# Kernel tuning notes

Hardware: AMD Instinct MI355X
Metric: run time of the kernel (lower is better)

The kernel has to match this reference:

```python
import jax, jax.numpy as jnp
import numpy as np

B, S, H = 2, 2048, 2048
NH, HD = 16, 128


def _rope_tables(seq_len, dim, base=10000.0):
    inv_freq = 1.0 / (base ** (np.arange(0, dim, 2, dtype=np.float32) / dim))
    t = np.arange(seq_len, dtype=np.float32)
    freqs = np.outer(t, inv_freq)                      # [S, dim/2]
    emb = np.concatenate([freqs, freqs], axis=-1)      # [S, dim] (HF convention)
    return jnp.asarray(np.cos(emb)), jnp.asarray(np.sin(emb))


def setup_inputs() -> dict:
    key = jax.random.key(0)
    k1, k2, k3, k4, k5 = jax.random.split(key, 5)
    hidden_states = jax.random.normal(k1, (B, S, H), dtype=jnp.float32)
    # additive causal mask, broadcast over heads: (B, 1, S, S)
    causal = jnp.tril(jnp.ones((S, S), dtype=bool))
    attention_mask = jnp.where(causal, 0.0, -1e9).astype(jnp.float32)
    attention_mask = jnp.broadcast_to(attention_mask[None, None], (B, 1, S, S))
    rope_cos, rope_sin = _rope_tables(S, HD)
    scale = 1.0 / np.sqrt(H)
    Wq = jax.random.normal(k2, (H, H), dtype=jnp.float32) * scale
    Wk = jax.random.normal(k3, (H, H), dtype=jnp.float32) * scale
    Wv = jax.random.normal(k4, (H, H), dtype=jnp.float32) * scale
    Wo = jax.random.normal(k5, (H, H), dtype=jnp.float32) * scale
    return dict(hidden_states=hidden_states, attention_mask=attention_mask,
                rope_cos=rope_cos, rope_sin=rope_sin, Wq=Wq, Wk=Wk, Wv=Wv, Wo=Wo)


def _rotate_half(x):
    half = x.shape[-1] // 2
    return jnp.concatenate([-x[..., half:], x[..., :half]], axis=-1)


def reference(hidden_states, attention_mask, rope_cos, rope_sin, Wq, Wk, Wv, Wo):
    bsz, q_len, _ = hidden_states.shape
    scaling = HD ** -0.5
    # projections (torch Linear: y = x @ W.T)
    q = (hidden_states @ Wq.T).reshape(bsz, q_len, NH, HD).transpose(0, 2, 1, 3)
    k = (hidden_states @ Wk.T).reshape(bsz, q_len, NH, HD).transpose(0, 2, 1, 3)
    v = (hidden_states @ Wv.T).reshape(bsz, q_len, NH, HD).transpose(0, 2, 1, 3)
    # RoPE (rotate_half convention)
    cos = rope_cos[None, None]  # [1,1,S,HD]
    sin = rope_sin[None, None]
    q = q * cos + _rotate_half(q) * sin
    k = k * cos + _rotate_half(k) * sin
    # attention
    scores = jnp.einsum('bhqd,bhkd->bhqk', q, k) * scaling + attention_mask
    attn = jax.nn.softmax(scores.astype(jnp.float32), axis=-1).astype(q.dtype)
    out = jnp.einsum('bhqk,bhkd->bhqd', attn, v)
    out = out.transpose(0, 2, 1, 3).reshape(bsz, q_len, NH * HD)
    return out @ Wo.T
```

## Files before the change

### kernel.cpp

```cpp
#include <hip/hip_runtime.h>
#include <hip/hip_bf16.h>

typedef __bf16 bf16;
typedef __attribute__((ext_vector_type(8))) __bf16 bf16x8;
typedef __attribute__((ext_vector_type(4))) __bf16 bf16x4;
typedef __attribute__((ext_vector_type(4))) float f32x4;

#define BB 2
#define SS 2048
#define HH 2048
#define NH 16
#define HD 128

#define GLOAD_LDS16(g, l)                                                  \
    __builtin_amdgcn_global_load_lds(                                      \
        (const __attribute__((address_space(1))) void*)(g),                \
        (__attribute__((address_space(3))) void*)(l), 16, 0, 0)

__global__ __launch_bounds__(256) void cast_all(const float* __restrict__ hs,
                                                const float* __restrict__ Wq,
                                                const float* __restrict__ Wk,
                                                const float* __restrict__ Wv,
                                                const float* __restrict__ Wo,
                                                bf16* __restrict__ Xb,
                                                bf16* __restrict__ Wqkv,
                                                bf16* __restrict__ Wob) {
    const int XE4 = (BB * SS * HH) / 4;
    const int WE4 = (HH * HH) / 4;
    int i = blockIdx.x * 256 + threadIdx.x;
    const float* src;
    bf16* dst;
    int off;
    if (i < XE4) { src = hs; dst = Xb; off = i; }
    else if (i < XE4 + WE4) { src = Wq; dst = Wqkv; off = i - XE4; }
    else if (i < XE4 + 2 * WE4) { src = Wk; dst = Wqkv + (size_t)HH * HH; off = i - XE4 - WE4; }
    else if (i < XE4 + 3 * WE4) { src = Wv; dst = Wqkv + 2 * (size_t)HH * HH; off = i - XE4 - 2 * WE4; }
    else { src = Wo; dst = Wob; off = i - XE4 - 3 * WE4; }
    f32x4 v = *reinterpret_cast<const f32x4*>(src + (size_t)off * 4);
    bf16x4 o;
    o[0] = (bf16)v[0]; o[1] = (bf16)v[1]; o[2] = (bf16)v[2]; o[3] = (bf16)v[3];
    *reinterpret_cast<bf16x4*>(dst + (size_t)off * 4) = o;
}

__global__ __launch_bounds__(512, 2) void gemm256_qkv(const bf16* __restrict__ A,
                                                      const bf16* __restrict__ B,
                                                      bf16* __restrict__ Cb,
                                                      int M, int N, int K) {
    __shared__ bf16 LA[2][256 * 64];
    __shared__ bf16 LB[2][256 * 64];
    const int tid = threadIdx.x, lane = tid & 63, wave = tid >> 6;
    const int l15 = lane & 15, lhi = lane >> 4;
    const int wr = wave >> 2, wc = wave & 3;
    const int NBY = M >> 8;
    const int cpx = gridDim.x >> 3;
    const int wg = (blockIdx.x & 7) * cpx + (blockIdx.x >> 3);
    const int m0 = (wg % NBY) * 256, n0 = (wg / NBY) * 256;
    const int NK = K >> 6;
    const int xorR = (l15 & 7) << 4;

    auto stageA = [&](int buf, int t, int h) {
        const int k0 = t << 6;
#pragma unroll
        for (int j = 0; j < 2; ++j) {
            int Xw = ((j * 128 + h * 64) << 7) + (wave << 10);
            int X = Xw + lane * 16;
            int T = X ^ (((X >> 7) & 7) << 4);
            GLOAD_LDS16(&A[(size_t)(m0 + (T >> 7)) * K + k0 + ((T & 127) >> 1)],
                        (char*)LA[buf] + Xw);
        }
    };
    auto stageB = [&](int buf, int t, int h) {
        const int k0 = t << 6;
#pragma unroll
        for (int j = 0; j < 2; ++j) {
            int base_row = h * 32 + (2 * j + (wave >> 2)) * 64;
            int Xw = (base_row << 7) + ((wave & 3) << 10);
            int X = Xw + lane * 16;
            int T = X ^ (((X >> 7) & 7) << 4);
            GLOAD_LDS16(&B[(size_t)(n0 + (T >> 7)) * K + k0 + ((T & 127) >> 1)],
                        (char*)LB[buf] + Xw);
        }
    };

    f32x4 acc[8][4] = {};

    stageA(0, 0, 0); stageB(0, 0, 0); stageB(0, 0, 1); stageA(0, 0, 1);
    stageA(1, 1, 0); stageB(1, 1, 1);
    asm volatile("s_waitcnt vmcnt(4)" ::: "memory");
    __builtin_amdgcn_s_barrier();

    bf16x8 af[4][2], bv0[2][2], bv1[2][2];

#pragma unroll 1
    for (int t = 0; t < NK; ++t) {
        const int buf = t & 1;
        char* lA = (char*)LA[buf];
        char* lB = (char*)LB[buf];

#pragma unroll
        for (int f = 0; f < 4; ++f)
#pragma unroll
            for (int ks = 0; ks < 2; ++ks) {
                int T = ((wr * 128 + f * 16 + l15) << 7) + ks * 64 + lhi * 16;
                af[f][ks] = *reinterpret_cast<const bf16x8*>(lA + (T ^ xorR));
            }
#pragma unroll
        for (int g = 0; g < 2; ++g)
#pragma unroll
            for (int ks = 0; ks < 2; ++ks) {
                int T = ((wc * 64 + g * 16 + l15) << 7) + ks * 64 + lhi * 16;
                bv0[g][ks] = *reinterpret_cast<const bf16x8*>(lB + (T ^ xorR));
            }
        if (t + 1 < NK) stageB(buf ^ 1, t + 1, 0);
        __builtin_amdgcn_s_barrier();
        __builtin_amdgcn_s_setprio(1);
#pragma unroll
        for (int f = 0; f < 4; ++f)
#pragma unroll
            for (int g = 0; g < 2; ++g)
#pragma unroll
                for (int ks = 0; ks < 2; ++ks)
                    acc[f][g] = __builtin_amdgcn_mfma_f32_16x16x32_bf16(af[f][ks], bv0[g][ks], acc[f][g], 0, 0, 0);
        __builtin_amdgcn_s_setprio(0);
        __builtin_amdgcn_s_barrier();

#pragma unroll
        for (int g = 0; g < 2; ++g)
#pragma unroll
            for (int ks = 0; ks < 2; ++ks) {
                int T = ((wc * 64 + 32 + g * 16 + l15) << 7) + ks * 64 + lhi * 16;
                bv1[g][ks] = *reinterpret_cast<const bf16x8*>(lB + (T ^ xorR));
            }
        if (t + 1 < NK) stageA(buf ^ 1, t + 1, 1);
        __builtin_amdgcn_s_barrier();
        __builtin_amdgcn_s_setprio(1);
#pragma unroll
        for (int f = 0; f < 4; ++f)
#pragma unroll
            for (int g = 0; g < 2; ++g)
#pragma unroll
                for (int ks = 0; ks < 2; ++ks)
                    acc[f][2 + g] = __builtin_amdgcn_mfma_f32_16x16x32_bf16(af[f][ks], bv1[g][ks], acc[f][2 + g], 0, 0, 0);
        __builtin_amdgcn_s_setprio(0);
        __builtin_amdgcn_s_barrier();

#pragma unroll
        for (int f = 0; f < 4; ++f)
#pragma unroll
            for (int ks = 0; ks < 2; ++ks) {
                int T = ((wr * 128 + 64 + f * 16 + l15) << 7) + ks * 64 + lhi * 16;
                af[f][ks] = *reinterpret_cast<const bf16x8*>(lA + (T ^ xorR));
            }
        if (t + 2 < NK) stageA(buf, t + 2, 0);
        __builtin_amdgcn_s_barrier();
        __builtin_amdgcn_s_setprio(1);
#pragma unroll
        for (int f = 0; f < 4; ++f)
#pragma unroll
            for (int g = 0; g < 2; ++g)
#pragma unroll
                for (int ks = 0; ks < 2; ++ks)
                    acc[4 + f][2 + g] = __builtin_amdgcn_mfma_f32_16x16x32_bf16(af[f][ks], bv1[g][ks], acc[4 + f][2 + g], 0, 0, 0);
        __builtin_amdgcn_s_setprio(0);
        __builtin_amdgcn_s_barrier();

        if (t + 2 < NK) stageB(buf, t + 2, 1);
        __builtin_amdgcn_s_barrier();
        __builtin_amdgcn_s_setprio(1);
#pragma unroll
        for (int f = 0; f < 4; ++f)
#pragma unroll
            for (int g = 0; g < 2; ++g)
#pragma unroll
                for (int ks = 0; ks < 2; ++ks)
                    acc[4 + f][g] = __builtin_amdgcn_mfma_f32_16x16x32_bf16(af[f][ks], bv0[g][ks], acc[4 + f][g], 0, 0, 0);
        __builtin_amdgcn_s_setprio(0);
        if (t + 2 == NK) {
            asm volatile("s_waitcnt vmcnt(0)" ::: "memory");
        } else if (t + 1 < NK) {
            asm volatile("s_waitcnt vmcnt(4)" ::: "memory");
        }
        __builtin_amdgcn_s_barrier();
    }

#pragma unroll
    for (int mf = 0; mf < 8; ++mf)
#pragma unroll
        for (int nf = 0; nf < 4; ++nf)
#pragma unroll
            for (int r = 0; r < 4; ++r) {
                int gm = m0 + wr * 128 + mf * 16 + lhi * 4 + r;
                int gn = n0 + wc * 64 + nf * 16 + l15;
                int proj = gn >> 11, n2 = gn & 2047;
                int b = gm >> 11, s = gm & (SS - 1);
                int h = n2 >> 7, d = n2 & (HD - 1);
                Cb[((size_t)proj << 23) + ((((size_t)(b * NH + h)) * SS + s) << 7) + d] =
                    (bf16)acc[mf][nf][r];
            }
}

__global__ __launch_bounds__(256) void gemm_bt(const bf16* __restrict__ A,
                                               const bf16* __restrict__ B,
                                               float* __restrict__ Cf,
                                               int M, int N, int K) {
    __shared__ bf16 As[128 * 64];
    __shared__ bf16 Bs[128 * 64];
    const int tid = threadIdx.x;
    const int lane = tid & 63, wave = tid >> 6;
    const int l15 = lane & 15, lhi = lane >> 4;
    const int m0 = blockIdx.y * 128, n0 = blockIdx.x * 128;
    const int wm = (wave >> 1) * 64, wn = (wave & 1) * 64;
    const int lrow = lane >> 3;
    const int lcol = (lane & 7) * 8;

    f32x4 acc[4][4] = {};

    for (int k0 = 0; k0 < K; k0 += 64) {
#pragma unroll
        for (int j = 0; j < 4; ++j) {
            const int c = wave * 4 + j;
            const int row = c * 8 + lrow;
            GLOAD_LDS16(&A[(size_t)(m0 + row) * K + k0 + lcol], &As[c * 512]);
            GLOAD_LDS16(&B[(size_t)(n0 + row) * K + k0 + lcol], &Bs[c * 512]);
        }
        __syncthreads();
#pragma unroll
        for (int ks = 0; ks < 2; ++ks) {
            bf16x8 af[4], bfr[4];
#pragma unroll
            for (int i = 0; i < 4; ++i)
                af[i] = *reinterpret_cast<const bf16x8*>(&As[(wm + i * 16 + l15) * 64 + ks * 32 + 8 * lhi]);
#pragma unroll
            for (int j = 0; j < 4; ++j)
                bfr[j] = *reinterpret_cast<const bf16x8*>(&Bs[(wn + j * 16 + l15) * 64 + ks * 32 + 8 * lhi]);
#pragma unroll
            for (int i = 0; i < 4; ++i)
#pragma unroll
                for (int j = 0; j < 4; ++j)
                    acc[i][j] = __builtin_amdgcn_mfma_f32_16x16x32_bf16(af[i], bfr[j], acc[i][j], 0, 0, 0);
        }
        __syncthreads();
    }

#pragma unroll
    for (int i = 0; i < 4; ++i)
#pragma unroll
        for (int j = 0; j < 4; ++j)
#pragma unroll
            for (int r = 0; r < 4; ++r) {
                int gm = m0 + wm + i * 16 + lhi * 4 + r;
                int gn = n0 + wn + j * 16 + l15;
                Cf[(size_t)gm * N + gn] = acc[i][j][r];
            }
}

__global__ __launch_bounds__(256) void rope_tv(bf16* __restrict__ Qh,
                                               bf16* __restrict__ Kh,
                                               const float* __restrict__ cosT,
                                               const float* __restrict__ sinT,
                                               const bf16* __restrict__ Vh,
                                               bf16* __restrict__ Vt) {
    __shared__ bf16 T[64 * 64];
    const int tid = threadIdx.x;
    if (blockIdx.x < 2048) {
        int idx = blockIdx.x * 256 + tid;
        int g = idx & 7;
        int s = (idx >> 3) & (SS - 1);
        int head = idx >> 14;
        int d0 = g * 8;
        size_t base = ((size_t)head * SS + s) * HD;
        f32x4 ca = *reinterpret_cast<const f32x4*>(&cosT[s * HD + d0]);
        f32x4 cb = *reinterpret_cast<const f32x4*>(&cosT[s * HD + d0 + 4]);
        f32x4 sa = *reinterpret_cast<const f32x4*>(&sinT[s * HD + d0]);
        f32x4 sb = *reinterpret_cast<const f32x4*>(&sinT[s * HD + d0 + 4]);
        bf16x8 ql = *reinterpret_cast<const bf16x8*>(&Qh[base + d0]);
        bf16x8 qh = *reinterpret_cast<const bf16x8*>(&Qh[base + 64 + d0]);
        bf16x8 kl = *reinterpret_cast<const bf16x8*>(&Kh[base + d0]);
        bf16x8 kh = *reinterpret_cast<const bf16x8*>(&Kh[base + 64 + d0]);
        bf16x8 qlo, qhi, klo, khi;
#pragma unroll
        for (int j = 0; j < 8; ++j) {
            float c = (j < 4) ? ca[j] : cb[j - 4];
            float sn = (j < 4) ? sa[j] : sb[j - 4];
            float q0 = (float)ql[j], q1 = (float)qh[j];
            float k0 = (float)kl[j], k1 = (float)kh[j];
            qlo[j] = (bf16)(q0 * c - q1 * sn);
            qhi[j] = (bf16)(q1 * c + q0 * sn);
            klo[j] = (bf16)(k0 * c - k1 * sn);
            khi[j] = (bf16)(k1 * c + k0 * sn);
        }
        *reinterpret_cast<bf16x8*>(&Qh[base + d0]) = qlo;
        *reinterpret_cast<bf16x8*>(&Qh[base + 64 + d0]) = qhi;
        *reinterpret_cast<bf16x8*>(&Kh[base + d0]) = klo;
        *reinterpret_cast<bf16x8*>(&Kh[base + 64 + d0]) = khi;
    } else {
        const int b2 = blockIdx.x - 2048;
        const int s0 = (b2 & 31) * 64;
        const int d0 = ((b2 >> 5) & 1) * 64;
        const int head = b2 >> 6;
        const bf16* src = Vh + ((size_t)head * SS) * HD;
        bf16* dst = Vt + ((size_t)head * HD) * SS;

#pragma unroll
        for (int i = 0; i < 2; ++i) {
            int id = tid + i * 256;
            int r = id >> 3, c16 = id & 7;
            bf16x8 v = *reinterpret_cast<const bf16x8*>(&src[(size_t)(s0 + r) * HD + d0 + c16 * 8]);
            int sw = c16 ^ ((r ^ (r >> 3)) & 7);
            *reinterpret_cast<bf16x8*>((char*)T + r * 128 + sw * 16) = v;
        }
        __syncthreads();
#pragma unroll
        for (int i = 0; i < 2; ++i) {
            int id = tid + i * 256;
            int dr = id >> 3, sc8 = (id & 7) * 8;
            bf16x8 o;
#pragma unroll
            for (int j = 0; j < 8; ++j) {
                int r = sc8 + j;
                int sw = (dr >> 3) ^ ((r ^ (r >> 3)) & 7);
                o[j] = *reinterpret_cast<const bf16*>((char*)T + r * 128 + sw * 16 + (dr & 7) * 2);
            }
            *reinterpret_cast<bf16x8*>(&dst[(size_t)(d0 + dr) * SS + s0 + sc8]) = o;
        }
    }
}

__global__ __launch_bounds__(512) void attn_kernel(const bf16* __restrict__ Q,
                                                   const bf16* __restrict__ K,
                                                   const bf16* __restrict__ Vt,
                                                   bf16* __restrict__ Ob) {
    __shared__ bf16 Ks[2][64 * 128];
    __shared__ bf16 Vs[2][128 * 64];
    __shared__ bf16 Ps[8][16 * 72];

    const int tid = threadIdx.x, lane = tid & 63, wave = tid >> 6;
    const int l15 = lane & 15, lhi = lane >> 4;
    const int bid = blockIdx.x;
    const int orig = (bid & 7) * 32 + (bid >> 3);
    const int head = orig >> 3;
    const int pi = orig & 7;
    const int b = head >> 4, h = head & (NH - 1);
    const size_t hb = (size_t)head * SS * HD;
    const bf16* Vth = Vt + (size_t)head * HD * SS;
    const float cexp = 0.08838834764831845f * 1.4426950408889634f;
    const float THR = 62.0f;

    auto stageKV = [&](int buf, int kv0) {
#pragma unroll
        for (int j = 0; j < 2; ++j) {
            int Xw = (j * 8 + wave) << 10;
            int X = Xw + lane * 16;
            int T = X ^ (((X >> 8) & 7) << 4);
            GLOAD_LDS16(&K[hb + (size_t)(kv0 + (T >> 8)) * HD + ((T & 255) >> 1)],
                        (char*)Ks[buf] + Xw);
        }
#pragma unroll
        for (int j = 0; j < 2; ++j) {
            int Xw = (j * 8 + wave) << 10;
            int X = Xw + lane * 16;
            int T = X ^ (((X >> 7) & 7) << 4);
            GLOAD_LDS16(&Vth[(size_t)(T >> 7) * SS + kv0 + ((T & 127) >> 1)],
                        (char*)Vs[buf] + Xw);
        }
    };

#pragma unroll 1
    for (int part = 0; part < 2; ++part) {
        const int t = part ? (15 - pi) : pi;
        const int q0 = t * 128;
        const int qw = q0 + wave * 16;
        const int nkv = 2 * t + 2;

        bf16x8 qf[4];
#pragma unroll
        for (int ks = 0; ks < 4; ++ks)
            qf[ks] = *reinterpret_cast<const bf16x8*>(
                &Q[hb + (size_t)(qw + l15) * HD + ks * 32 + 8 * lhi]);

        f32x4 oacc[8] = {};
        float Mr[4], Lp[4];
#pragma unroll
        for (int r = 0; r < 4; ++r) { Mr[r] = -INFINITY; Lp[r] = 0.f; }

        stageKV(0, 0);
        asm volatile("s_waitcnt vmcnt(0)" ::: "memory");
        __builtin_amdgcn_s_barrier();

        for (int it = 0; it < nkv; ++it) {
            const int cur = it & 1;
            if (it + 1 < nkv) stageKV(cur ^ 1, (it + 1) * 64);

            f32x4 sf[4] = {};
#pragma unroll
            for (int ks = 0; ks < 4; ++ks) {
#pragma unroll
                for (int ne = 0; ne < 4; ++ne) {
                    int row = ne * 16 + l15;
                    bf16x8 kf = *reinterpret_cast<const bf16x8*>(
                        (const char*)Ks[cur] + ((row * 256 + (ks * 4 + lhi) * 16) ^ ((row & 7) << 4)));
                    sf[ne] = __builtin_amdgcn_mfma_f32_16x16x32_bf16(qf[ks], kf, sf[ne], 0, 0, 0);
                }
            }

            if (it >= nkv - 2) {
#pragma unroll
                for (int ne = 0; ne < 4; ++ne)
#pragma unroll
                    for (int r = 0; r < 4; ++r) {
                        int gq = qw + lhi * 4 + r;
                        int gk = it * 64 + ne * 16 + l15;
                        if (gk > gq) sf[ne][r] = -INFINITY;
                    }
            }

            float lm[4];
#pragma unroll
            for (int r = 0; r < 4; ++r)
                lm[r] = fmaxf(fmaxf(sf[0][r], sf[1][r]), fmaxf(sf[2][r], sf[3][r]));
            bool need = (lm[0] > Mr[0] + THR) || (lm[1] > Mr[1] + THR) ||
                        (lm[2] > Mr[2] + THR) || (lm[3] > Mr[3] + THR);
            if (__any(need)) {
                float rmax[4] = {lm[0], lm[1], lm[2], lm[3]};
#pragma unroll
                for (int m = 1; m < 16; m <<= 1)
#pragma unroll
                    for (int r = 0; r < 4; ++r)
                        rmax[r] = fmaxf(rmax[r], __shfl_xor(rmax[r], m));
#pragma unroll
                for (int r = 0; r < 4; ++r) {
                    float nM = fmaxf(Mr[r], rmax[r]);
                    float scf = __builtin_amdgcn_exp2f((Mr[r] - nM) * cexp);
                    Mr[r] = nM;
                    Lp[r] *= scf;
#pragma unroll
                    for (int nf = 0; nf < 8; ++nf) oacc[nf][r] *= scf;
                }
            }
#pragma unroll
            for (int ne = 0; ne < 4; ++ne)
#pragma unroll
                for (int r = 0; r < 4; ++r) {
                    float p = __builtin_amdgcn_exp2f((sf[ne][r] - Mr[r]) * cexp);
                    Lp[r] += p;
                    Ps[wave][(lhi * 4 + r) * 72 + ne * 16 + l15] = (bf16)p;
                }

#pragma unroll
            for (int ks = 0; ks < 2; ++ks) {
                bf16x8 pa = *reinterpret_cast<const bf16x8*>(
                    &Ps[wave][l15 * 72 + ks * 32 + 8 * lhi]);
#pragma unroll
                for (int nf = 0; nf < 8; ++nf) {
                    int row = nf * 16 + l15;
                    bf16x8 vb = *reinterpret_cast<const bf16x8*>(
                        (const char*)Vs[cur] + ((row * 128 + (ks * 4 + lhi) * 16) ^ ((row & 7) << 4)));
                    oacc[nf] = __builtin_amdgcn_mfma_f32_16x16x32_bf16(pa, vb, oacc[nf], 0, 0, 0);
                }
            }

            asm volatile("s_waitcnt vmcnt(0)" ::: "memory");
            __builtin_amdgcn_s_barrier();
        }

#pragma unroll
        for (int m = 1; m < 16; m <<= 1)
#pragma unroll
            for (int r = 0; r < 4; ++r)
                Lp[r] += __shfl_xor(Lp[r], m);
        float inv[4];
#pragma unroll
        for (int r = 0; r < 4; ++r) inv[r] = 1.f / Lp[r];
#pragma unroll
        for (int nf = 0; nf < 8; ++nf)
#pragma unroll
            for (int r = 0; r < 4; ++r) {
                int s = qw + lhi * 4 + r;
                int d = nf * 16 + l15;
                Ob[((size_t)(b * SS + s)) * HH + h * HD + d] = (bf16)(oacc[nf][r] * inv[r]);
            }
    }
}

extern "C" void kernel_launch(void* const* d_in, const int* in_sizes, int n_in,
                              void* d_out, int out_size, void* d_ws, size_t ws_size,
                              hipStream_t stream) {
    const float* hs   = (const float*)d_in[0];
    const float* cosT = (const float*)d_in[2];
    const float* sinT = (const float*)d_in[3];
    const float* Wq   = (const float*)d_in[4];
    const float* Wk   = (const float*)d_in[5];
    const float* Wv   = (const float*)d_in[6];
    const float* Wo   = (const float*)d_in[7];
    float* out = (float*)d_out;

    char* w = (char*)d_ws;
    auto alloc = [&](size_t bytes) {
        char* p = w;
        w += (bytes + 255) & ~(size_t)255;
        return p;
    };
    const size_t XE = (size_t)BB * SS * HH;
    const size_t WE = (size_t)HH * HH;
    bf16* Xb   = (bf16*)alloc(XE * 2);
    bf16* Wqkv = (bf16*)alloc(3 * WE * 2);
    bf16* Wob  = (bf16*)alloc(WE * 2);
    bf16* QKV  = (bf16*)alloc(3 * XE * 2);
    bf16* Vtg  = (bf16*)alloc(XE * 2);
    bf16* Ob   = (bf16*)alloc(XE * 2);

    const int M = BB * SS;
    bf16* Qh = QKV;
    bf16* Kh = QKV + XE;
    bf16* Vh = QKV + 2 * XE;

    {
        int total4 = (int)((XE + 4 * WE) / 4);
        cast_all<<<(total4 + 255) / 256, 256, 0, stream>>>(hs, Wq, Wk, Wv, Wo, Xb, Wqkv, Wob);
    }

    gemm256_qkv<<<dim3((M / 256) * (3 * HH / 256)), 512, 0, stream>>>(Xb, Wqkv, QKV, M, 3 * HH, HH);

    rope_tv<<<4096, 256, 0, stream>>>(Qh, Kh, cosT, sinT, Vh, Vtg);

    attn_kernel<<<256, 512, 0, stream>>>(Qh, Kh, Vtg, Ob);

    dim3 ogrid(HH / 128, M / 128);
    gemm_bt<<<ogrid, 256, 0, stream>>>(Ob, Wob, out, M, HH, HH);
}
```

Measured before the change: 273.8 us.

## Retile QKV GEMM to 256x192 blocks for balanced wave count

Changes the QKV projection GEMM tile from 256x256 to 256x192, giving 512 workgroups instead of 384 so the grid divides evenly across the CUs. The LDS staging of B, the MFMA phase schedule (three 16-column slices per wave instead of four), the vmcnt waits and the epilogue are reworked for the new shape. This trades slightly lower arithmetic intensity per tile for avoiding a partially filled last wave.

```diff
diff --git a/kernel.cpp b/kernel.cpp
--- a/kernel.cpp
+++ b/kernel.cpp
@@ -47,14 +47,14 @@
                                                       bf16* __restrict__ Cb,
                                                       int M, int N, int K) {
     __shared__ bf16 LA[2][256 * 64];
-    __shared__ bf16 LB[2][256 * 64];
+    __shared__ bf16 LB[2][192 * 64];
     const int tid = threadIdx.x, lane = tid & 63, wave = tid >> 6;
     const int l15 = lane & 15, lhi = lane >> 4;
     const int wr = wave >> 2, wc = wave & 3;
     const int NBY = M >> 8;
     const int cpx = gridDim.x >> 3;
     const int wg = (blockIdx.x & 7) * cpx + (blockIdx.x >> 3);
-    const int m0 = (wg % NBY) * 256, n0 = (wg / NBY) * 256;
+    const int m0 = (wg & 15) * 256, n0 = (wg >> 4) * 192;
     const int NK = K >> 6;
     const int xorR = (l15 & 7) << 4;
 
@@ -62,34 +62,33 @@
         const int k0 = t << 6;
 #pragma unroll
         for (int j = 0; j < 2; ++j) {
-            int Xw = ((j * 128 + h * 64) << 7) + (wave << 10);
+            int Xw = (h * 128 + j * 64 + wave * 8) << 7;
             int X = Xw + lane * 16;
             int T = X ^ (((X >> 7) & 7) << 4);
             GLOAD_LDS16(&A[(size_t)(m0 + (T >> 7)) * K + k0 + ((T & 127) >> 1)],
                         (char*)LA[buf] + Xw);
         }
     };
-    auto stageB = [&](int buf, int t, int h) {
+    auto stageB = [&](int buf, int t, int s) {
         const int k0 = t << 6;
-#pragma unroll
-        for (int j = 0; j < 2; ++j) {
-            int base_row = h * 32 + (2 * j + (wave >> 2)) * 64;
-            int Xw = (base_row << 7) + ((wave & 3) << 10);
-            int X = Xw + lane * 16;
-            int T = X ^ (((X >> 7) & 7) << 4);
-            GLOAD_LDS16(&B[(size_t)(n0 + (T >> 7)) * K + k0 + ((T & 127) >> 1)],
-                        (char*)LB[buf] + Xw);
-        }
+        int row_base = (wave >> 1) * 48 + s * 16 + (wave & 1) * 8;
+        int Xw = row_base << 7;
+        int X = Xw + lane * 16;
+        int T = X ^ (((X >> 7) & 7) << 4);
+        GLOAD_LDS16(&B[(size_t)(n0 + (T >> 7)) * K + k0 + ((T & 127) >> 1)],
+                    (char*)LB[buf] + Xw);
     };
 
-    f32x4 acc[8][4] = {};
-
-    stageA(0, 0, 0); stageB(0, 0, 0); stageB(0, 0, 1); stageA(0, 0, 1);
-    stageA(1, 1, 0); stageB(1, 1, 1);
-    asm volatile("s_waitcnt vmcnt(4)" ::: "memory");
+    f32x4 acc[8][3] = {};
+
+    stageA(0, 0, 0); stageA(0, 0, 1);
+    stageB(0, 0, 0); stageB(0, 0, 1); stageB(0, 0, 2);
+    stageA(1, 1, 0); stageA(1, 1, 1);
+    stageB(1, 1, 0); stageB(1, 1, 1);
+    asm volatile("s_waitcnt vmcnt(6)" ::: "memory");
     __builtin_amdgcn_s_barrier();
 
-    bf16x8 af[4][2], bv0[2][2], bv1[2][2];
+    bf16x8 af[8][2], bv[2];
 
 #pragma unroll 1
     for (int t = 0; t < NK; ++t) {
@@ -98,87 +97,62 @@
         char* lB = (char*)LB[buf];
 
 #pragma unroll
-        for (int f = 0; f < 4; ++f)
+        for (int mf = 0; mf < 8; ++mf)
 #pragma unroll
             for (int ks = 0; ks < 2; ++ks) {
-                int T = ((wr * 128 + f * 16 + l15) << 7) + ks * 64 + lhi * 16;
-                af[f][ks] = *reinterpret_cast<const bf16x8*>(lA + (T ^ xorR));
-            }
-#pragma unroll
-        for (int g = 0; g < 2; ++g)
-#pragma unroll
-            for (int ks = 0; ks < 2; ++ks) {
-                int T = ((wc * 64 + g * 16 + l15) << 7) + ks * 64 + lhi * 16;
-                bv0[g][ks] = *reinterpret_cast<const bf16x8*>(lB + (T ^ xorR));
-            }
-        if (t + 1 < NK) stageB(buf ^ 1, t + 1, 0);
+                int T = ((wr * 128 + mf * 16 + l15) << 7) + ks * 64 + lhi * 16;
+                af[mf][ks] = *reinterpret_cast<const bf16x8*>(lA + (T ^ xorR));
+            }
+#pragma unroll
+        for (int ks = 0; ks < 2; ++ks) {
+            int T = ((wc * 48 + l15) << 7) + ks * 64 + lhi * 16;
+            bv[ks] = *reinterpret_cast<const bf16x8*>(lB + (T ^ xorR));
+        }
+        if (t + 1 < NK) stageB(buf ^ 1, t + 1, 2);
         __builtin_amdgcn_s_barrier();
         __builtin_amdgcn_s_setprio(1);
 #pragma unroll
-        for (int f = 0; f < 4; ++f)
-#pragma unroll
-            for (int g = 0; g < 2; ++g)
-#pragma unroll
-                for (int ks = 0; ks < 2; ++ks)
-                    acc[f][g] = __builtin_amdgcn_mfma_f32_16x16x32_bf16(af[f][ks], bv0[g][ks], acc[f][g], 0, 0, 0);
+        for (int mf = 0; mf < 8; ++mf)
+#pragma unroll
+            for (int ks = 0; ks < 2; ++ks)
+                acc[mf][0] = __builtin_amdgcn_mfma_f32_16x16x32_bf16(af[mf][ks], bv[ks], acc[mf][0], 0, 0, 0);
         __builtin_amdgcn_s_setprio(0);
         __builtin_amdgcn_s_barrier();
 
 #pragma unroll
-        for (int g = 0; g < 2; ++g)
-#pragma unroll
-            for (int ks = 0; ks < 2; ++ks) {
-                int T = ((wc * 64 + 32 + g * 16 + l15) << 7) + ks * 64 + lhi * 16;
-                bv1[g][ks] = *reinterpret_cast<const bf16x8*>(lB + (T ^ xorR));
-            }
-        if (t + 1 < NK) stageA(buf ^ 1, t + 1, 1);
+        for (int ks = 0; ks < 2; ++ks) {
+            int T = ((wc * 48 + 16 + l15) << 7) + ks * 64 + lhi * 16;
+            bv[ks] = *reinterpret_cast<const bf16x8*>(lB + (T ^ xorR));
+        }
+        if (t + 2 < NK) { stageB(buf, t + 2, 0); stageA(buf, t + 2, 0); }
         __builtin_amdgcn_s_barrier();
         __builtin_amdgcn_s_setprio(1);
 #pragma unroll
-        for (int f = 0; f < 4; ++f)
-#pragma unroll
-            for (int g = 0; g < 2; ++g)
-#pragma unroll
-                for (int ks = 0; ks < 2; ++ks)
-                    acc[f][2 + g] = __builtin_amdgcn_mfma_f32_16x16x32_bf16(af[f][ks], bv1[g][ks], acc[f][2 + g], 0, 0, 0);
+        for (int mf = 0; mf < 8; ++mf)
+#pragma unroll
+            for (int ks = 0; ks < 2; ++ks)
+                acc[mf][1] = __builtin_amdgcn_mfma_f32_16x16x32_bf16(af[mf][ks], bv[ks], acc[mf][1], 0, 0, 0);
         __builtin_amdgcn_s_setprio(0);
         __builtin_amdgcn_s_barrier();
 
 #pragma unroll
-        for (int f = 0; f < 4; ++f)
-#pragma unroll
-            for (int ks = 0; ks < 2; ++ks) {
-                int T = ((wr * 128 + 64 + f * 16 + l15) << 7) + ks * 64 + lhi * 16;
-                af[f][ks] = *reinterpret_cast<const bf16x8*>(lA + (T ^ xorR));
-            }
-        if (t + 2 < NK) stageA(buf, t + 2, 0);
+        for (int ks = 0; ks < 2; ++ks) {
+            int T = ((wc * 48 + 32 + l15) << 7) + ks * 64 + lhi * 16;
+            bv[ks] = *reinterpret_cast<const bf16x8*>(lB + (T ^ xorR));
+        }
+        if (t + 2 < NK) { stageB(buf, t + 2, 1); stageA(buf, t + 2, 1); }
         __builtin_amdgcn_s_barrier();
         __builtin_amdgcn_s_setprio(1);
 #pragma unroll
-        for (int f = 0; f < 4; ++f)
-#pragma unroll
-            for (int g = 0; g < 2; ++g)
-#pragma unroll
-                for (int ks = 0; ks < 2; ++ks)
-                    acc[4 + f][2 + g] = __builtin_amdgcn_mfma_f32_16x16x32_bf16(af[f][ks], bv1[g][ks], acc[4 + f][2 + g], 0, 0, 0);
+        for (int mf = 0; mf < 8; ++mf)
+#pragma unroll
+            for (int ks = 0; ks < 2; ++ks)
+                acc[mf][2] = __builtin_amdgcn_mfma_f32_16x16x32_bf16(af[mf][ks], bv[ks], acc[mf][2], 0, 0, 0);
         __builtin_amdgcn_s_setprio(0);
-        __builtin_amdgcn_s_barrier();
-
-        if (t + 2 < NK) stageB(buf, t + 2, 1);
-        __builtin_amdgcn_s_barrier();
-        __builtin_amdgcn_s_setprio(1);
-#pragma unroll
-        for (int f = 0; f < 4; ++f)
-#pragma unroll
-            for (int g = 0; g < 2; ++g)
-#pragma unroll
-                for (int ks = 0; ks < 2; ++ks)
-                    acc[4 + f][g] = __builtin_amdgcn_mfma_f32_16x16x32_bf16(af[f][ks], bv0[g][ks], acc[4 + f][g], 0, 0, 0);
-        __builtin_amdgcn_s_setprio(0);
-        if (t + 2 == NK) {
+        if (t + 2 < NK) {
+            asm volatile("s_waitcnt vmcnt(6)" ::: "memory");
+        } else if (t + 2 == NK) {
             asm volatile("s_waitcnt vmcnt(0)" ::: "memory");
-        } else if (t + 1 < NK) {
-            asm volatile("s_waitcnt vmcnt(4)" ::: "memory");
         }
         __builtin_amdgcn_s_barrier();
     }
@@ -186,16 +160,16 @@
 #pragma unroll
     for (int mf = 0; mf < 8; ++mf)
 #pragma unroll
-        for (int nf = 0; nf < 4; ++nf)
+        for (int nsl = 0; nsl < 3; ++nsl)
 #pragma unroll
             for (int r = 0; r < 4; ++r) {
                 int gm = m0 + wr * 128 + mf * 16 + lhi * 4 + r;
-                int gn = n0 + wc * 64 + nf * 16 + l15;
+                int gn = n0 + wc * 48 + nsl * 16 + l15;
                 int proj = gn >> 11, n2 = gn & 2047;
                 int b = gm >> 11, s = gm & (SS - 1);
                 int h = n2 >> 7, d = n2 & (HD - 1);
                 Cb[((size_t)proj << 23) + ((((size_t)(b * NH + h)) * SS + s) << 7) + d] =
-                    (bf16)acc[mf][nf][r];
+                    (bf16)acc[mf][nsl][r];
             }
 }
 
@@ -519,7 +493,7 @@
         cast_all<<<(total4 + 255) / 256, 256, 0, stream>>>(hs, Wq, Wk, Wv, Wo, Xb, Wqkv, Wob);
     }
 
-    gemm256_qkv<<<dim3((M / 256) * (3 * HH / 256)), 512, 0, stream>>>(Xb, Wqkv, QKV, M, 3 * HH, HH);
+    gemm256_qkv<<<512, 512, 0, stream>>>(Xb, Wqkv, QKV, M, 3 * HH, HH);
 
     rope_tv<<<4096, 256, 0, stream>>>(Qh, Kh, cosT, sinT, Vh, Vtg);
 
```

Measured after the change: 261.3 us. 4.5% less time.
